# Kernel optimization log

Hardware: AMD Instinct MI355X
Metric: run time of the kernel (lower is better)

Reference implementation:

```python
import jax, jax.numpy as jnp
import numpy as np


def setup_inputs() -> dict:
    key = jax.random.key(0)
    ks = jax.random.split(key, 8)
    B = 65536
    scale = lambda fan_in: 1.0 / np.sqrt(fan_in)
    return {
        "x": jax.random.normal(ks[0], (B, 784), dtype=jnp.float32),
        "w0": jax.random.normal(ks[1], (124, 784), dtype=jnp.float32) * scale(784),
        "w1": jax.random.normal(ks[2], (32, 124), dtype=jnp.float32) * scale(124),
        "w3": jax.random.normal(ks[3], (22, 32), dtype=jnp.float32) * scale(32),
        "b3": jax.random.normal(ks[4], (22,), dtype=jnp.float32) * scale(32),
        "w5": jax.random.normal(ks[5], (21, 22), dtype=jnp.float32) * scale(22),
        "b5": jax.random.normal(ks[6], (21,), dtype=jnp.float32) * scale(22),
        "w7": jax.random.normal(ks[7], (10, 21), dtype=jnp.float32) * scale(21),
    }


def reference(x, w0, w1, w3, b3, w5, b5, w7):
    # x: [B, 784]; PyTorch Linear: y = x @ W.T (+ b)
    h = x @ w0.T                       # [B, 124] (no bias, no activation)
    h = jax.nn.relu(h @ w1.T)          # [B, 32]
    h = jax.nn.relu(h @ w3.T + b3)     # [B, 22]
    h = jax.nn.relu(h @ w5.T + b5)     # [B, 21]
    logits = h @ w7.T                  # [B, 10]
    return jax.nn.log_softmax(logits, axis=1)
```

## Files before the change

### kernel.cpp

```cpp
#include <hip/hip_runtime.h>
#include <hip/hip_fp16.h>

typedef _Float16 half8 __attribute__((ext_vector_type(8)));
typedef __fp16 cvt2_t __attribute__((ext_vector_type(2)));
typedef float f32x4 __attribute__((ext_vector_type(4)));

#define W0F_UNITS (13 * 1024)
#define W1F_OFF   (W0F_UNITS * 16)
#define W1F_UNITS 512
#define SW_OFF    (W1F_OFF + W1F_UNITS * 16)

#define L_H0   0
#define L_H1   8192
#define L_H3   0
#define L_H5   3200
#define L_OS   6400
#define LDS_SZ 10240

__global__ void prep_weights(const float* __restrict__ w0,
                             const float* __restrict__ w1,
                             const float* __restrict__ w3,
                             const float* __restrict__ b3,
                             const float* __restrict__ w5,
                             const float* __restrict__ b5,
                             const float* __restrict__ w7,
                             char* __restrict__ ws) {
  int tid = blockIdx.x * 256 + threadIdx.x;
  if (tid < W0F_UNITS) {
    int t  = tid >> 10;
    int kf = (tid >> 9) & 1;
    int nf = (tid >> 6) & 7;
    int l  = tid & 63;
    int n  = nf * 16 + (l & 15);
    int k0 = t * 64 + kf * 32 + (l >> 4) * 8;
    alignas(16) __half h[8];
#pragma unroll
    for (int e = 0; e < 8; e++) {
      int k = k0 + e;
      h[e] = __float2half((n < 124 && k < 784) ? w0[n * 784 + k] : 0.f);
    }
    *(uint4*)(ws + tid * 16) = *(const uint4*)h;
    return;
  }
  int r = tid - W0F_UNITS;
  if (r < W1F_UNITS) {
    int kf = r >> 7;
    int nf = (r >> 6) & 1;
    int l  = r & 63;
    int n  = nf * 16 + (l & 15);
    int k0 = kf * 32 + (l >> 4) * 8;
    alignas(16) __half h[8];
#pragma unroll
    for (int e = 0; e < 8; e++) {
      int k = k0 + e;
      h[e] = __float2half((k < 124) ? w1[n * 124 + k] : 0.f);
    }
    *(uint4*)(ws + W1F_OFF + r * 16) = *(const uint4*)h;
    return;
  }
  r -= W1F_UNITS;
  float* sw = (float*)(ws + SW_OFF);
  if (r < 704) { sw[r] = w3[r]; return; }
  r -= 704;
  if (r < 504) {
    int n = r / 24, k = r % 24;
    sw[704 + r] = (k < 22) ? w5[n * 22 + k] : 0.f;
    return;
  }
  r -= 504;
  if (r < 240) {
    int n = r / 24, k = r % 24;
    sw[1208 + r] = (k < 21) ? w7[n * 21 + k] : 0.f;
    return;
  }
  r -= 240;
  if (r < 24) { sw[1448 + r] = (r < 22) ? b3[r] : 0.f; return; }
  r -= 24;
  if (r < 24) { sw[1472 + r] = (r < 21) ? b5[r] : 0.f; return; }
}

__device__ __forceinline__ half8 cvt8(const float4& a, const float4& b) {
  cvt2_t p0 = __builtin_amdgcn_cvt_pkrtz(a.x, a.y);
  cvt2_t p1 = __builtin_amdgcn_cvt_pkrtz(a.z, a.w);
  cvt2_t p2 = __builtin_amdgcn_cvt_pkrtz(b.x, b.y);
  cvt2_t p3 = __builtin_amdgcn_cvt_pkrtz(b.z, b.w);
  uint4 u;
  u.x = __builtin_bit_cast(unsigned, p0);
  u.y = __builtin_bit_cast(unsigned, p1);
  u.z = __builtin_bit_cast(unsigned, p2);
  u.w = __builtin_bit_cast(unsigned, p3);
  return __builtin_bit_cast(half8, u);
}

__global__ __launch_bounds__(64, 2) void fused_mlp(
    const float* __restrict__ x, const char* __restrict__ ws,
    float* __restrict__ out) {
  __shared__ alignas(16) char sm[LDS_SZ];
  const int l  = threadIdx.x;
  const int lr = l & 15;
  const int lg = l >> 4;
  const size_t row0 = (size_t)blockIdx.x * 32;

  const float* xb0 = x + (row0 + lr) * 784;
  const float* xb1 = xb0 + 16 * 784;

  f32x4 acc[2][8];
#pragma unroll
  for (int mf = 0; mf < 2; mf++)
#pragma unroll
    for (int nf = 0; nf < 8; nf++) acc[mf][nf] = f32x4{0.f, 0.f, 0.f, 0.f};

  const uint4* wf = (const uint4*)ws;

  float4 xA[2][2][2], xB[2][2][2];

#pragma unroll
  for (int mf = 0; mf < 2; mf++)
#pragma unroll
    for (int kf = 0; kf < 2; kf++) {
      const float* p = (mf ? xb1 : xb0) + kf * 32 + lg * 8;
      xA[mf][kf][0] = *(const float4*)p;
      xA[mf][kf][1] = *(const float4*)(p + 4);
    }

#define TILE_BODY(T, XC, XN, PF_FULL)                                          \
  {                                                                            \
    half8 bf[2][8];                                                            \
    _Pragma("unroll") for (int kf = 0; kf < 2; kf++)                           \
        _Pragma("unroll") for (int nf = 0; nf < 8; nf++)                       \
            bf[kf][nf] = __builtin_bit_cast(                                   \
                half8, wf[(T) * 1024 + kf * 512 + nf * 64 + l]);               \
    half8 af[2][2];                                                            \
    _Pragma("unroll") for (int mf = 0; mf < 2; mf++)                           \
        _Pragma("unroll") for (int kf = 0; kf < 2; kf++)                       \
            af[mf][kf] = cvt8(XC[mf][kf][0], XC[mf][kf][1]);                   \
    if (PF_FULL) {                                                             \
      _Pragma("unroll") for (int mf = 0; mf < 2; mf++)                         \
          _Pragma("unroll") for (int kf = 0; kf < 2; kf++) {                   \
        const float* p = (mf ? xb1 : xb0) + ((T) + 1) * 64 + kf * 32 + lg * 8; \
        XN[mf][kf][0] = *(const float4*)p;                                     \
        XN[mf][kf][1] = *(const float4*)(p + 4);                               \
      }                                                                        \
    } else {                \
      const float4 z = {0.f, 0.f, 0.f, 0.f};                                   \
      _Pragma("unroll") for (int mf = 0; mf < 2; mf++) {                       \
        const float* p = (mf ? xb1 : xb0) + 768 + lg * 8;                      \
        bool v = (lg < 2);                                                     \
        XN[mf][0][0] = v ? *(const float4*)p : z;                              \
        XN[mf][0][1] = v ? *(const float4*)(p + 4) : z;                        \
        XN[mf][1][0] = z;                                                      \
        XN[mf][1][1] = z;                                                      \
      }                                                                        \
    }                                                                          \
    _Pragma("unroll") for (int kf = 0; kf < 2; kf++)                           \
        _Pragma("unroll") for (int mf = 0; mf < 2; mf++)                       \
            _Pragma("unroll") for (int nf = 0; nf < 8; nf++)                   \
                acc[mf][nf] = __builtin_amdgcn_mfma_f32_16x16x32_f16(          \
                    af[mf][kf], bf[kf][nf], acc[mf][nf], 0, 0, 0);             \
  }

  TILE_BODY(0, xA, xB, 1)
  TILE_BODY(1, xB, xA, 1)
  TILE_BODY(2, xA, xB, 1)
  TILE_BODY(3, xB, xA, 1)
  TILE_BODY(4, xA, xB, 1)
  TILE_BODY(5, xB, xA, 1)
  TILE_BODY(6, xA, xB, 1)
  TILE_BODY(7, xB, xA, 1)
  TILE_BODY(8, xA, xB, 1)
  TILE_BODY(9, xB, xA, 1)
  TILE_BODY(10, xA, xB, 1)
  TILE_BODY(11, xB, xA, 0)

  {
    half8 bf[8];
#pragma unroll
    for (int nf = 0; nf < 8; nf++)
      bf[nf] = __builtin_bit_cast(half8, wf[12 * 1024 + nf * 64 + l]);
    half8 af[2];
#pragma unroll
    for (int mf = 0; mf < 2; mf++) af[mf] = cvt8(xA[mf][0][0], xA[mf][0][1]);
#pragma unroll
    for (int mf = 0; mf < 2; mf++)
#pragma unroll
      for (int nf = 0; nf < 8; nf++)
        acc[mf][nf] = __builtin_amdgcn_mfma_f32_16x16x32_f16(
            af[mf], bf[nf], acc[mf][nf], 0, 0, 0);
  }

  half8 b1[4][2];
  {
    const uint4* w1f = (const uint4*)(ws + W1F_OFF);
#pragma unroll
    for (int kf = 0; kf < 4; kf++)
#pragma unroll
      for (int nf = 0; nf < 2; nf++)
        b1[kf][nf] = __builtin_bit_cast(half8, w1f[kf * 128 + nf * 64 + l]);
  }

#pragma unroll
  for (int mf = 0; mf < 2; mf++)
#pragma unroll
    for (int nf = 0; nf < 8; nf++)
#pragma unroll
      for (int q = 0; q < 4; q++) {
        int rr = mf * 16 + lg * 4 + q;
        int cc = nf * 16 + lr;
        *(__half*)(sm + L_H0 + rr * 256 + ((2 * cc) ^ ((rr & 7) << 4))) =
            __float2half(acc[mf][nf][q]);
      }
  __syncthreads();

  f32x4 acc1[2][2];
#pragma unroll
  for (int mf = 0; mf < 2; mf++) {
    acc1[mf][0] = f32x4{0.f, 0.f, 0.f, 0.f};
    acc1[mf][1] = f32x4{0.f, 0.f, 0.f, 0.f};
  }
#pragma unroll
  for (int kf = 0; kf < 4; kf++) {
    half8 a1[2];
#pragma unroll
    for (int mf = 0; mf < 2; mf++) {
      int rr = mf * 16 + lr;
      int cb = kf * 64 + lg * 16;
      a1[mf] = *(const half8*)(sm + L_H0 + rr * 256 + (cb ^ ((rr & 7) << 4)));
    }
#pragma unroll
    for (int mf = 0; mf < 2; mf++)
#pragma unroll
      for (int nf = 0; nf < 2; nf++)
        acc1[mf][nf] = __builtin_amdgcn_mfma_f32_16x16x32_f16(
            a1[mf], b1[kf][nf], acc1[mf][nf], 0, 0, 0);
  }
#pragma unroll
  for (int mf = 0; mf < 2; mf++)
#pragma unroll
    for (int nf = 0; nf < 2; nf++)
#pragma unroll
      for (int q = 0; q < 4; q++) {
        int rr = mf * 16 + lg * 4 + q;
        int cc = nf * 16 + lr;
        float v = fmaxf(acc1[mf][nf][q], 0.f);
        *(__half*)(sm + L_H1 + rr * 64 + ((2 * cc) ^ ((rr & 3) << 4))) =
            __float2half(v);
      }
  __syncthreads();

  const int r = l & 31;
  const int j = l >> 5;
  float h1v[32];
#pragma unroll
  for (int cb = 0; cb < 4; cb++) {
    half8 v = *(const half8*)(sm + L_H1 + r * 64 + ((cb * 16) ^ ((r & 3) << 4)));
#pragma unroll
    for (int e = 0; e < 8; e++) h1v[cb * 8 + e] = (float)v[e];
  }
  const float* w3g = (const float*)(ws + SW_OFF);
  const float* w5g = (const float*)(ws + SW_OFF + 2816);
  const float* w7g = (const float*)(ws + SW_OFF + 4832);
  const float* b3g = (const float*)(ws + SW_OFF + 5792);
  const float* b5g = (const float*)(ws + SW_OFF + 5888);
  float* h3l = (float*)(sm + L_H3);
  float* h5l = (float*)(sm + L_H5);

#pragma unroll
  for (int i = 0; i < 11; i++) {
    int n = j + 2 * i;
    float s = b3g[n];
    const float4* wrow = (const float4*)(w3g + n * 32);
#pragma unroll
    for (int kk = 0; kk < 8; kk++) {
      float4 wv = wrow[kk];
      s += h1v[4 * kk] * wv.x + h1v[4 * kk + 1] * wv.y +
           h1v[4 * kk + 2] * wv.z + h1v[4 * kk + 3] * wv.w;
    }
    h3l[r * 25 + n] = fmaxf(s, 0.f);
  }
  __syncthreads();
  float h3v[24];
#pragma unroll
  for (int k = 0; k < 24; k++) h3v[k] = (k < 22) ? h3l[r * 25 + k] : 0.f;
#pragma unroll
  for (int i = 0; i < 11; i++) {
    int n = j + 2 * i;
    if (n < 21) {
      float s = b5g[n];
      const float4* wrow = (const float4*)(w5g + n * 24);
#pragma unroll
      for (int kk = 0; kk < 6; kk++) {
        float4 wv = wrow[kk];
        s += h3v[4 * kk] * wv.x + h3v[4 * kk + 1] * wv.y +
             h3v[4 * kk + 2] * wv.z + h3v[4 * kk + 3] * wv.w;
      }
      h5l[r * 25 + n] = fmaxf(s, 0.f);
    }
  }
  __syncthreads();
  if (j == 0) {
    float h5v[24];
#pragma unroll
    for (int k = 0; k < 24; k++) h5v[k] = (k < 21) ? h5l[r * 25 + k] : 0.f;
    float lgt[10];
    float mx = -3.4e38f;
#pragma unroll
    for (int n = 0; n < 10; n++) {
      float s = 0.f;
      const float4* wrow = (const float4*)(w7g + n * 24);
#pragma unroll
      for (int kk = 0; kk < 6; kk++) {
        float4 wv = wrow[kk];
        s += h5v[4 * kk] * wv.x + h5v[4 * kk + 1] * wv.y +
             h5v[4 * kk + 2] * wv.z + h5v[4 * kk + 3] * wv.w;
      }
      lgt[n] = s;
      mx = fmaxf(mx, s);
    }
    float se = 0.f;
#pragma unroll
    for (int n = 0; n < 10; n++) se += __expf(lgt[n] - mx);
    const float lse = mx + __logf(se);
    float* os = (float*)(sm + L_OS);
#pragma unroll
    for (int n = 0; n < 10; n++) os[r * 10 + n] = lgt[n] - lse;
  }
  __syncthreads();
  {
    const float* os = (const float*)(sm + L_OS);
#pragma unroll
    for (int i = 0; i < 5; i++) out[row0 * 10 + i * 64 + l] = os[i * 64 + l];
  }
}

extern "C" void kernel_launch(void* const* d_in, const int* in_sizes, int n_in,
                              void* d_out, int out_size, void* d_ws, size_t ws_size,
                              hipStream_t stream) {
  const float* x  = (const float*)d_in[0];
  const float* w0 = (const float*)d_in[1];
  const float* w1 = (const float*)d_in[2];
  const float* w3 = (const float*)d_in[3];
  const float* b3 = (const float*)d_in[4];
  const float* w5 = (const float*)d_in[5];
  const float* b5 = (const float*)d_in[6];
  const float* w7 = (const float*)d_in[7];
  float* out = (float*)d_out;
  char* ws = (char*)d_ws;

  const int prep_threads = W0F_UNITS + W1F_UNITS + 704 + 504 + 240 + 24 + 24;
  prep_weights<<<(prep_threads + 255) / 256, 256, 0, stream>>>(w0, w1, w3, b3,
                                                               w5, b5, w7, ws);
  fused_mlp<<<65536 / 32, 64, 0, stream>>>(x, ws, out);
}
```

Before: 57.32 us.

## Stage x tiles through swizzled LDS with coalesced nontemporal row loads

The first-layer input loads now read contiguous 64-float row segments per lane group and use nontemporal loads. Each segment is converted to fp16 and written into a double-buffered, XOR-swizzled LDS tile, then read back in MFMA fragment layout, instead of loading fragment-shaped 32-byte chunks straight from global memory. Weight fragments are preloaded one tile ahead into registers. The aim is better coalescing of the dominant x stream, at the cost of extra LDS traffic and a larger LDS footprint (18 KB).

```diff
diff --git a/kernel.cpp b/kernel.cpp
--- a/kernel.cpp
+++ b/kernel.cpp
@@ -10,12 +10,13 @@
 #define W1F_UNITS 512
 #define SW_OFF    (W1F_OFF + W1F_UNITS * 16)
 
-#define L_H0   0
-#define L_H1   8192
+#define L_XT   0
+#define L_H0   8192
+#define L_H1   16384
 #define L_H3   0
 #define L_H5   3200
 #define L_OS   6400
-#define LDS_SZ 10240
+#define LDS_SZ 18432
 
 __global__ void prep_weights(const float* __restrict__ w0,
                              const float* __restrict__ w1,
@@ -79,19 +80,6 @@
   if (r < 24) { sw[1472 + r] = (r < 21) ? b5[r] : 0.f; return; }
 }
 
-__device__ __forceinline__ half8 cvt8(const float4& a, const float4& b) {
-  cvt2_t p0 = __builtin_amdgcn_cvt_pkrtz(a.x, a.y);
-  cvt2_t p1 = __builtin_amdgcn_cvt_pkrtz(a.z, a.w);
-  cvt2_t p2 = __builtin_amdgcn_cvt_pkrtz(b.x, b.y);
-  cvt2_t p3 = __builtin_amdgcn_cvt_pkrtz(b.z, b.w);
-  uint4 u;
-  u.x = __builtin_bit_cast(unsigned, p0);
-  u.y = __builtin_bit_cast(unsigned, p1);
-  u.z = __builtin_bit_cast(unsigned, p2);
-  u.w = __builtin_bit_cast(unsigned, p3);
-  return __builtin_bit_cast(half8, u);
-}
-
 __global__ __launch_bounds__(64, 2) void fused_mlp(
     const float* __restrict__ x, const char* __restrict__ ws,
     float* __restrict__ out) {
@@ -101,8 +89,12 @@
   const int lg = l >> 4;
   const size_t row0 = (size_t)blockIdx.x * 32;
 
-  const float* xb0 = x + (row0 + lr) * 784;
-  const float* xb1 = xb0 + 16 * 784;
+  const float* xcol = x + (row0 + lg) * 784 + lr * 4;
+
+  const int wb0 = lg * 128 + ((lr * 8) ^ (lg << 4));
+  const int wb1 = wb0 ^ 64;
+  const int rb0 = lr * 128 + ((lg * 16) ^ ((lr & 7) << 4));
+  const int rb1 = lr * 128 + ((64 + lg * 16) ^ ((lr & 7) << 4));
 
   f32x4 acc[2][8];
 #pragma unroll
@@ -112,80 +104,66 @@
 
   const uint4* wf = (const uint4*)ws;
 
-  float4 xA[2][2][2], xB[2][2][2];
-
-#pragma unroll
-  for (int mf = 0; mf < 2; mf++)
-#pragma unroll
-    for (int kf = 0; kf < 2; kf++) {
-      const float* p = (mf ? xb1 : xb0) + kf * 32 + lg * 8;
-      xA[mf][kf][0] = *(const float4*)p;
-      xA[mf][kf][1] = *(const float4*)(p + 4);
-    }
-
-#define TILE_BODY(T, XC, XN, PF_FULL)                                          \
+  f32x4 xr[8];
+  half8 bfr[2][8];
+
+#define XLOAD(T, GUARD)                                                        \
   {                                                                            \
-    half8 bf[2][8];                                                            \
-    _Pragma("unroll") for (int kf = 0; kf < 2; kf++)                           \
-        _Pragma("unroll") for (int nf = 0; nf < 8; nf++)                       \
-            bf[kf][nf] = __builtin_bit_cast(                                   \
-                half8, wf[(T) * 1024 + kf * 512 + nf * 64 + l]);               \
-    half8 af[2][2];                                                            \
-    _Pragma("unroll") for (int mf = 0; mf < 2; mf++)                           \
-        _Pragma("unroll") for (int kf = 0; kf < 2; kf++)                       \
-            af[mf][kf] = cvt8(XC[mf][kf][0], XC[mf][kf][1]);                   \
-    if (PF_FULL) {                                                             \
-      _Pragma("unroll") for (int mf = 0; mf < 2; mf++)                         \
-          _Pragma("unroll") for (int kf = 0; kf < 2; kf++) {                   \
-        const float* p = (mf ? xb1 : xb0) + ((T) + 1) * 64 + kf * 32 + lg * 8; \
-        XN[mf][kf][0] = *(const float4*)p;                                     \
-        XN[mf][kf][1] = *(const float4*)(p + 4);                               \
-      }                                                                        \
-    } else {                \
-      const float4 z = {0.f, 0.f, 0.f, 0.f};                                   \
-      _Pragma("unroll") for (int mf = 0; mf < 2; mf++) {                       \
-        const float* p = (mf ? xb1 : xb0) + 768 + lg * 8;                      \
-        bool v = (lg < 2);                                                     \
-        XN[mf][0][0] = v ? *(const float4*)p : z;                              \
-        XN[mf][0][1] = v ? *(const float4*)(p + 4) : z;                        \
-        XN[mf][1][0] = z;                                                      \
-        XN[mf][1][1] = z;                                                      \
-      }                                                                        \
+    const float* pt = xcol + (size_t)(T) * 64;                                 \
+    _Pragma("unroll") for (int i = 0; i < 8; i++) {                            \
+      if (!(GUARD) || lr < 4)                                                  \
+        xr[i] = __builtin_nontemporal_load((const f32x4*)(pt + i * 3136));     \
+      else                                                                     \
+        xr[i] = f32x4{0.f, 0.f, 0.f, 0.f};                                     \
     }                                                                          \
-    _Pragma("unroll") for (int kf = 0; kf < 2; kf++)                           \
-        _Pragma("unroll") for (int mf = 0; mf < 2; mf++)                       \
-            _Pragma("unroll") for (int nf = 0; nf < 8; nf++)                   \
-                acc[mf][nf] = __builtin_amdgcn_mfma_f32_16x16x32_f16(          \
-                    af[mf][kf], bf[kf][nf], acc[mf][nf], 0, 0, 0);             \
-  }
-
-  TILE_BODY(0, xA, xB, 1)
-  TILE_BODY(1, xB, xA, 1)
-  TILE_BODY(2, xA, xB, 1)
-  TILE_BODY(3, xB, xA, 1)
-  TILE_BODY(4, xA, xB, 1)
-  TILE_BODY(5, xB, xA, 1)
-  TILE_BODY(6, xA, xB, 1)
-  TILE_BODY(7, xB, xA, 1)
-  TILE_BODY(8, xA, xB, 1)
-  TILE_BODY(9, xB, xA, 1)
-  TILE_BODY(10, xA, xB, 1)
-  TILE_BODY(11, xB, xA, 0)
-
-  {
-    half8 bf[8];
-#pragma unroll
-    for (int nf = 0; nf < 8; nf++)
-      bf[nf] = __builtin_bit_cast(half8, wf[12 * 1024 + nf * 64 + l]);
-    half8 af[2];
-#pragma unroll
-    for (int mf = 0; mf < 2; mf++) af[mf] = cvt8(xA[mf][0][0], xA[mf][0][1]);
-#pragma unroll
-    for (int mf = 0; mf < 2; mf++)
-#pragma unroll
-      for (int nf = 0; nf < 8; nf++)
-        acc[mf][nf] = __builtin_amdgcn_mfma_f32_16x16x32_f16(
-            af[mf], bf[nf], acc[mf][nf], 0, 0, 0);
+  }
+
+#define XSTORE(PAR)                                                            \
+  {                                                                            \
+    _Pragma("unroll") for (int i = 0; i < 8; i++) {                            \
+      cvt2_t q0 = __builtin_amdgcn_cvt_pkrtz(xr[i][0], xr[i][1]);              \
+      cvt2_t q1 = __builtin_amdgcn_cvt_pkrtz(xr[i][2], xr[i][3]);              \
+      uint2 u;                                                                 \
+      u.x = __builtin_bit_cast(unsigned, q0);                                  \
+      u.y = __builtin_bit_cast(unsigned, q1);                                  \
+      *(uint2*)(sm + L_XT + (PAR) * 4096 + ((i & 1) ? wb1 : wb0) + i * 512) =  \
+          u;                                                                   \
+    }                                                                          \
+  }
+
+#define BFLOAD(T)                                                              \
+  _Pragma("unroll") for (int kf = 0; kf < 2; kf++)                             \
+      _Pragma("unroll") for (int nf = 0; nf < 8; nf++)                         \
+          bfr[kf][nf] = __builtin_bit_cast(                                    \
+              half8, wf[(T) * 1024 + kf * 512 + nf * 64 + l]);
+
+  XLOAD(0, false)
+  BFLOAD(0)
+  XSTORE(0)
+
+#pragma unroll
+  for (int T = 0; T < 13; T++) {
+    const int par = T & 1;
+    if (T < 12) XLOAD(T + 1, (T + 1) == 12)
+    {
+      half8 af[2][2];
+      af[0][0] = *(const half8*)(sm + L_XT + par * 4096 + rb0);
+      af[1][0] = *(const half8*)(sm + L_XT + par * 4096 + rb0 + 2048);
+      af[0][1] = *(const half8*)(sm + L_XT + par * 4096 + rb1);
+      af[1][1] = *(const half8*)(sm + L_XT + par * 4096 + rb1 + 2048);
+#pragma unroll
+      for (int kf = 0; kf < 2; kf++)
+#pragma unroll
+        for (int mf = 0; mf < 2; mf++)
+#pragma unroll
+          for (int nf = 0; nf < 8; nf++)
+            acc[mf][nf] = __builtin_amdgcn_mfma_f32_16x16x32_f16(
+                af[mf][kf], bfr[kf][nf], acc[mf][nf], 0, 0, 0);
+    }
+    if (T < 12) {
+      BFLOAD(T + 1)
+      XSTORE(par ^ 1)
+    }
   }
 
   half8 b1[4][2];
```

Result: slower. 68.57 us (+19.6%).

## Deepen x prefetch to two tiles ahead and prefetch weight fragments

Applied to the files above, without the earlier changes.

Restructures the first-layer K loop so x tiles are loaded two tiles ahead (double-buffered xP/xQ) and the weight fragments for the next tile are loaded right after the current tile's MFMAs are issued. The last partial tile now runs through the same body, with zero padding on the second K half. The goal is to hide global-memory latency for both x and weights behind MFMA work. It raises register pressure, since more loads are in flight, which could cause spills under launch_bounds(64,2).

```diff
diff --git a/kernel.cpp b/kernel.cpp
--- a/kernel.cpp
+++ b/kernel.cpp
@@ -79,11 +79,11 @@
   if (r < 24) { sw[1472 + r] = (r < 21) ? b5[r] : 0.f; return; }
 }
 
-__device__ __forceinline__ half8 cvt8(const float4& a, const float4& b) {
-  cvt2_t p0 = __builtin_amdgcn_cvt_pkrtz(a.x, a.y);
-  cvt2_t p1 = __builtin_amdgcn_cvt_pkrtz(a.z, a.w);
-  cvt2_t p2 = __builtin_amdgcn_cvt_pkrtz(b.x, b.y);
-  cvt2_t p3 = __builtin_amdgcn_cvt_pkrtz(b.z, b.w);
+__device__ __forceinline__ half8 cvt8(const f32x4& a, const f32x4& b) {
+  cvt2_t p0 = __builtin_amdgcn_cvt_pkrtz(a[0], a[1]);
+  cvt2_t p1 = __builtin_amdgcn_cvt_pkrtz(a[2], a[3]);
+  cvt2_t p2 = __builtin_amdgcn_cvt_pkrtz(b[0], b[1]);
+  cvt2_t p3 = __builtin_amdgcn_cvt_pkrtz(b[2], b[3]);
   uint4 u;
   u.x = __builtin_bit_cast(unsigned, p0);
   u.y = __builtin_bit_cast(unsigned, p1);
@@ -112,81 +112,60 @@
 
   const uint4* wf = (const uint4*)ws;
 
-  float4 xA[2][2][2], xB[2][2][2];
-
-#pragma unroll
-  for (int mf = 0; mf < 2; mf++)
-#pragma unroll
-    for (int kf = 0; kf < 2; kf++) {
-      const float* p = (mf ? xb1 : xb0) + kf * 32 + lg * 8;
-      xA[mf][kf][0] = *(const float4*)p;
-      xA[mf][kf][1] = *(const float4*)(p + 4);
-    }
-
-#define TILE_BODY(T, XC, XN, PF_FULL)                                          \
+  f32x4 xP[2][2][2], xQ[2][2][2];
+  half8 bfr[2][8];
+
+#define XLOAD(T, B, G)                                                         \
   {                                                                            \
-    half8 bf[2][8];                                                            \
-    _Pragma("unroll") for (int kf = 0; kf < 2; kf++)                           \
-        _Pragma("unroll") for (int nf = 0; nf < 8; nf++)                       \
-            bf[kf][nf] = __builtin_bit_cast(                                   \
-                half8, wf[(T) * 1024 + kf * 512 + nf * 64 + l]);               \
+    _Pragma("unroll") for (int mf = 0; mf < 2; mf++)                           \
+        _Pragma("unroll") for (int kf = 0; kf < 2; kf++) {                     \
+      const float* p = (mf ? xb1 : xb0) + (T) * 64 + kf * 32 + lg * 8;         \
+      if (!(G) || (kf == 0 && lg < 2)) {                                       \
+        B[mf][kf][0] = *(const f32x4*)p;                                       \
+        B[mf][kf][1] = *(const f32x4*)(p + 4);                                 \
+      } else {                                                                 \
+        B[mf][kf][0] = f32x4{0.f, 0.f, 0.f, 0.f};                              \
+        B[mf][kf][1] = f32x4{0.f, 0.f, 0.f, 0.f};                              \
+      }                                                                        \
+    }                                                                          \
+  }
+
+#define BF(T)                                                                  \
+  _Pragma("unroll") for (int kf = 0; kf < 2; kf++)                             \
+      _Pragma("unroll") for (int nf = 0; nf < 8; nf++)                         \
+          bfr[kf][nf] = __builtin_bit_cast(                                    \
+              half8, wf[(T) * 1024 + kf * 512 + nf * 64 + l]);
+
+#define BODY(B)                                                                \
+  {                                                                            \
     half8 af[2][2];                                                            \
     _Pragma("unroll") for (int mf = 0; mf < 2; mf++)                           \
         _Pragma("unroll") for (int kf = 0; kf < 2; kf++)                       \
-            af[mf][kf] = cvt8(XC[mf][kf][0], XC[mf][kf][1]);                   \
-    if (PF_FULL) {                                                             \
-      _Pragma("unroll") for (int mf = 0; mf < 2; mf++)                         \
-          _Pragma("unroll") for (int kf = 0; kf < 2; kf++) {                   \
-        const float* p = (mf ? xb1 : xb0) + ((T) + 1) * 64 + kf * 32 + lg * 8; \
-        XN[mf][kf][0] = *(const float4*)p;                                     \
-        XN[mf][kf][1] = *(const float4*)(p + 4);                               \
-      }                                                                        \
-    } else {                \
-      const float4 z = {0.f, 0.f, 0.f, 0.f};                                   \
-      _Pragma("unroll") for (int mf = 0; mf < 2; mf++) {                       \
-        const float* p = (mf ? xb1 : xb0) + 768 + lg * 8;                      \
-        bool v = (lg < 2);                                                     \
-        XN[mf][0][0] = v ? *(const float4*)p : z;                              \
-        XN[mf][0][1] = v ? *(const float4*)(p + 4) : z;                        \
-        XN[mf][1][0] = z;                                                      \
-        XN[mf][1][1] = z;                                                      \
-      }                                                                        \
-    }                                                                          \
+            af[mf][kf] = cvt8(B[mf][kf][0], B[mf][kf][1]);                     \
     _Pragma("unroll") for (int kf = 0; kf < 2; kf++)                           \
         _Pragma("unroll") for (int mf = 0; mf < 2; mf++)                       \
             _Pragma("unroll") for (int nf = 0; nf < 8; nf++)                   \
                 acc[mf][nf] = __builtin_amdgcn_mfma_f32_16x16x32_f16(          \
-                    af[mf][kf], bf[kf][nf], acc[mf][nf], 0, 0, 0);             \
-  }
-
-  TILE_BODY(0, xA, xB, 1)
-  TILE_BODY(1, xB, xA, 1)
-  TILE_BODY(2, xA, xB, 1)
-  TILE_BODY(3, xB, xA, 1)
-  TILE_BODY(4, xA, xB, 1)
-  TILE_BODY(5, xB, xA, 1)
-  TILE_BODY(6, xA, xB, 1)
-  TILE_BODY(7, xB, xA, 1)
-  TILE_BODY(8, xA, xB, 1)
-  TILE_BODY(9, xB, xA, 1)
-  TILE_BODY(10, xA, xB, 1)
-  TILE_BODY(11, xB, xA, 0)
-
-  {
-    half8 bf[8];
-#pragma unroll
-    for (int nf = 0; nf < 8; nf++)
-      bf[nf] = __builtin_bit_cast(half8, wf[12 * 1024 + nf * 64 + l]);
-    half8 af[2];
-#pragma unroll
-    for (int mf = 0; mf < 2; mf++) af[mf] = cvt8(xA[mf][0][0], xA[mf][0][1]);
-#pragma unroll
-    for (int mf = 0; mf < 2; mf++)
-#pragma unroll
-      for (int nf = 0; nf < 8; nf++)
-        acc[mf][nf] = __builtin_amdgcn_mfma_f32_16x16x32_f16(
-            af[mf], bf[nf], acc[mf][nf], 0, 0, 0);
-  }
+                    af[mf][kf], bfr[kf][nf], acc[mf][nf], 0, 0, 0);            \
+  }
+
+  XLOAD(0, xP, 0)
+  BF(0)
+  XLOAD(1, xQ, 0)
+
+  BODY(xP) BF(1)  XLOAD(2, xP, 0)
+  BODY(xQ) BF(2)  XLOAD(3, xQ, 0)
+  BODY(xP) BF(3)  XLOAD(4, xP, 0)
+  BODY(xQ) BF(4)  XLOAD(5, xQ, 0)
+  BODY(xP) BF(5)  XLOAD(6, xP, 0)
+  BODY(xQ) BF(6)  XLOAD(7, xQ, 0)
+  BODY(xP) BF(7)  XLOAD(8, xP, 0)
+  BODY(xQ) BF(8)  XLOAD(9, xQ, 0)
+  BODY(xP) BF(9)  XLOAD(10, xP, 0)
+  BODY(xQ) BF(10) XLOAD(11, xQ, 0)
+  BODY(xP) BF(11) XLOAD(12, xP, 1)
+  BODY(xQ) BF(12)
+  BODY(xP)
 
   half8 b1[4][2];
   {
```

Result: no change. 57.62 us (+0.5%).
